# Kernel optimization log

Hardware: AMD Instinct MI355X
Metric: run time of the kernel (lower is better)

The kernel has to match this reference:

```python
import jax, jax.numpy as jnp
import numpy as np

NEG_SLOPE = 0.2  # PyG GATConv default negative_slope
NUM_GRAPHS = 64


def gat_conv(x, src, dst, W, a_src, a_dst, bias, concat):
    """PyG-style GATConv (eval mode, self-loops already appended to src/dst)."""
    N = x.shape[0]
    H, C = a_src.shape
    h = (x @ W).reshape(N, H, C)                      # [N,H,C]
    al_s = jnp.sum(h * a_src, axis=-1)                # [N,H]
    al_d = jnp.sum(h * a_dst, axis=-1)                # [N,H]
    e = jax.nn.leaky_relu(al_s[src] + al_d[dst], NEG_SLOPE)  # [E,H]
    # numerically-stable segment softmax over incoming edges of each dst node
    m = jax.ops.segment_max(e, dst, num_segments=N)   # [N,H]
    ex = jnp.exp(e - m[dst])
    denom = jax.ops.segment_sum(ex, dst, num_segments=N)
    alpha = ex / (denom[dst] + 1e-16)                 # [E,H]
    out = jax.ops.segment_sum(h[src] * alpha[:, :, None], dst, num_segments=N)  # [N,H,C]
    out = out.reshape(N, H * C) if concat else out.mean(axis=1)
    return out + bias


def setup_inputs() -> dict:
    key = jax.random.key(0)
    ks = jax.random.split(key, 32)
    N, E, F_in, H = 20000, 100000, 128, 8
    x = jax.random.normal(ks[0], (N, F_in), jnp.float32)
    edge_index = jax.random.randint(ks[1], (2, E), 0, N, dtype=jnp.int32)
    batch = jnp.sort(jax.random.randint(ks[2], (N,), 0, NUM_GRAPHS, dtype=jnp.int32))
    inp = {"x": x, "edge_index": edge_index, "batch": batch}
    # (fan_in, per-head channels) for conv1..conv_final
    dims = [(F_in, 64), (512, 256), (2048, 256), (2048, 256), (2048, 256)]
    ki = 3
    for i, (fi, c) in enumerate(dims, 1):
        concat = i < 5
        inp[f"W{i}"] = jax.random.normal(ks[ki], (fi, H * c), jnp.float32) * (1.0 / np.sqrt(fi)); ki += 1
        inp[f"a_src{i}"] = jax.random.normal(ks[ki], (H, c), jnp.float32) * 0.1; ki += 1
        inp[f"a_dst{i}"] = jax.random.normal(ks[ki], (H, c), jnp.float32) * 0.1; ki += 1
        inp[f"b{i}"] = jnp.zeros((H * c if concat else c,), jnp.float32)
    inp["W_lin"] = jax.random.normal(ks[ki], (256, 128), jnp.float32) * (1.0 / np.sqrt(256))
    inp["b_lin"] = jnp.zeros((128,), jnp.float32)
    return inp


def reference(x, edge_index, batch,
              W1, a_src1, a_dst1, b1,
              W2, a_src2, a_dst2, b2,
              W3, a_src3, a_dst3, b3,
              W4, a_src4, a_dst4, b4,
              W5, a_src5, a_dst5, b5,
              W_lin, b_lin):
    N = x.shape[0]
    loop = jnp.arange(N, dtype=edge_index.dtype)  # GATConv add_self_loops=True
    src = jnp.concatenate([edge_index[0], loop])
    dst = jnp.concatenate([edge_index[1], loop])
    h = jax.nn.elu(gat_conv(x, src, dst, W1, a_src1, a_dst1, b1, True))
    h = jax.nn.elu(gat_conv(h, src, dst, W2, a_src2, a_dst2, b2, True))
    h = jax.nn.elu(gat_conv(h, src, dst, W3, a_src3, a_dst3, b3, True))
    h = jax.nn.elu(gat_conv(h, src, dst, W4, a_src4, a_dst4, b4, True))
    h = jax.nn.elu(gat_conv(h, src, dst, W5, a_src5, a_dst5, b5, False))
    sums = jax.ops.segment_sum(h, batch, num_segments=NUM_GRAPHS)
    counts = jax.ops.segment_sum(jnp.ones((N, 1), h.dtype), batch, num_segments=NUM_GRAPHS)
    pooled = jax.nn.elu(sums / jnp.maximum(counts, 1.0))  # global_mean_pool + elu
    return pooled @ W_lin + b_lin
```

## Files before the change

kernel.cpp:

```cpp
#include <hip/hip_runtime.h>
#include <hip/hip_fp16.h>
#include <math.h>

#define NHEADS 8
#define NG 64

typedef _Float16 half8_t __attribute__((ext_vector_type(8)));
typedef _Float16 half4_t __attribute__((ext_vector_type(4)));
typedef float    float4_t __attribute__((ext_vector_type(4)));
typedef __attribute__((address_space(1))) const void g_void;
typedef __attribute__((address_space(3))) void l_void;

__device__ __forceinline__ float elu_f(float x)   { return x > 0.f ? x : expf(x) - 1.f; }
__device__ __forceinline__ float lrelu_f(float x) { return x >= 0.f ? x : 0.2f * x; }

__device__ __forceinline__ float4 ld4(const float* p) { return *(const float4*)p; }
__device__ __forceinline__ float4 ld4(const __half* p) {
    const __half2* q = (const __half2*)p;
    __half2 a = q[0], b = q[1];
    return make_float4(__half2float(a.x), __half2float(a.y),
                       __half2float(b.x), __half2float(b.y));
}
__device__ __forceinline__ void st4(float* p, float4 v) { *(float4*)p = v; }
__device__ __forceinline__ void st4(__half* p, float4 v) {
    __half2 a, b;
    a.x = __float2half(v.x); a.y = __float2half(v.y);
    b.x = __float2half(v.z); b.y = __float2half(v.w);
    __half2* q = (__half2*)p; q[0] = a; q[1] = b;
}
__device__ __forceinline__ float scl(float v)  { return v; }
__device__ __forceinline__ float scl(__half v) { return __half2float(v); }
__device__ __forceinline__ void sst(float* p, float v)  { *p = v; }
__device__ __forceinline__ void sst(__half* p, float v) { *p = __float2half(v); }

struct h4s { __half a, b, c, d; };

__global__ void hist_kernel(const int* __restrict__ ei, int E, int Etot, int* __restrict__ counts) {
    int e = blockIdx.x * blockDim.x + threadIdx.x;
    if (e >= Etot) return;
    int dst = (e < E) ? ei[E + e] : (e - E);
    atomicAdd(&counts[dst], 1);
}

__global__ __launch_bounds__(256) void scan_kernel(const int* __restrict__ counts,
                                                   int* __restrict__ offsets,
                                                   int* __restrict__ cursor, int N) {
    __shared__ int wsum[4];
    const int tid = threadIdx.x;
    const int lane = tid & 63, wid = tid >> 6;
    int carry = 0;
    for (int base = 0; base < N; base += 1024) {
        int i0 = base + tid * 4;
        int v0 = 0, v1 = 0, v2 = 0, v3 = 0;
        if (i0 + 3 < N) {
            int4 q = *(const int4*)(counts + i0);
            v0 = q.x; v1 = q.y; v2 = q.z; v3 = q.w;
        } else {
            if (i0     < N) v0 = counts[i0];
            if (i0 + 1 < N) v1 = counts[i0 + 1];
            if (i0 + 2 < N) v2 = counts[i0 + 2];
            if (i0 + 3 < N) v3 = counts[i0 + 3];
        }
        int tsum = v0 + v1 + v2 + v3;
        int incl = tsum;
#pragma unroll
        for (int off = 1; off < 64; off <<= 1) {
            int t = __shfl_up(incl, off);
            if (lane >= off) incl += t;
        }
        if (lane == 63) wsum[wid] = incl;
        __syncthreads();
        int woff = carry;
        for (int w = 0; w < wid; ++w) woff += wsum[w];
        int o0 = woff + incl - tsum;
        int o1 = o0 + v0, o2 = o1 + v1, o3 = o2 + v2;
        if (i0     < N) { offsets[i0]     = o0; cursor[i0]     = o0; }
        if (i0 + 1 < N) { offsets[i0 + 1] = o1; cursor[i0 + 1] = o1; }
        if (i0 + 2 < N) { offsets[i0 + 2] = o2; cursor[i0 + 2] = o2; }
        if (i0 + 3 < N) { offsets[i0 + 3] = o3; cursor[i0 + 3] = o3; }
        __syncthreads();
        carry += wsum[0] + wsum[1] + wsum[2] + wsum[3];
    }
    if (tid == 0) offsets[N] = carry;
}

__global__ void scatter_kernel(const int* __restrict__ ei, int E, int Etot,
                               int* __restrict__ cursor, int* __restrict__ perm_src) {
    int e = blockIdx.x * blockDim.x + threadIdx.x;
    if (e >= Etot) return;
    int src, dst;
    if (e < E) { src = ei[e]; dst = ei[E + e]; }
    else       { src = e - E; dst = e - E; }
    int pos = atomicAdd(&cursor[dst], 1);
    perm_src[pos] = src;
}

struct PrepArgs {
    const float* x; __half* x16; long n4;
    const float* W0; const float* W1; const float* W2; const float* W3; const float* W4;
    __half* T0; __half* T1; __half* T2; __half* T3; __half* T4;
    int K0, K1, K2, K3, K4;
    int N0, N1, N2, N3, N4;
    int b0, b1, b2, b3, b4, b5;
};

__global__ __launch_bounds__(256) void prep_kernel(PrepArgs a) {
    int bid = blockIdx.x;
    if (bid < a.b0) {
        long i = (long)bid * 256 + threadIdx.x;
        if (i < a.n4) {
            float4 v = ((const float4*)a.x)[i];
            h4s o; o.a = __float2half(v.x); o.b = __float2half(v.y);
            o.c = __float2half(v.z); o.d = __float2half(v.w);
            ((h4s*)a.x16)[i] = o;
        }
        return;
    }
    const float* W; __half* T; int K, Nn, t;
    if      (bid < a.b1) { W = a.W0; T = a.T0; K = a.K0; Nn = a.N0; t = bid - a.b0; }
    else if (bid < a.b2) { W = a.W1; T = a.T1; K = a.K1; Nn = a.N1; t = bid - a.b1; }
    else if (bid < a.b3) { W = a.W2; T = a.T2; K = a.K2; Nn = a.N2; t = bid - a.b2; }
    else if (bid < a.b4) { W = a.W3; T = a.T3; K = a.K3; Nn = a.N3; t = bid - a.b3; }
    else                 { W = a.W4; T = a.T4; K = a.K4; Nn = a.N4; t = bid - a.b4; }
    int tilesx = Nn >> 5;
    int nb = (t % tilesx) * 32, kb = (t / tilesx) * 32;
    __shared__ float tt[32][33];
    int tx = threadIdx.x & 31, ty = threadIdx.x >> 5;
#pragma unroll
    for (int r = 0; r < 32; r += 8)
        tt[ty + r][tx] = W[(size_t)(kb + ty + r) * Nn + nb + tx];
    __syncthreads();
#pragma unroll
    for (int r = 0; r < 32; r += 8)
        T[(size_t)(nb + ty + r) * K + kb + tx] = __float2half(tt[tx][ty + r]);
}

__global__ __launch_bounds__(256) void gemm_mfma_kernel(const __half* __restrict__ A,
                                                        const __half* __restrict__ Bt,
                                                        __half* __restrict__ C,
                                                        int M, int N, int K) {
    __shared__ __align__(16) __half Asm[128 * 64];
    __shared__ __align__(16) __half Bsm[128 * 64];
    const int tid  = threadIdx.x;
    const int lane = tid & 63;
    const int wave = tid >> 6;

    const int nwg = (int)(gridDim.x * gridDim.y);
    const int lin = (int)(blockIdx.y * gridDim.x + blockIdx.x);
    const int q = nwg >> 3, r = nwg & 7;
    const int xcd = lin & 7, idx = lin >> 3;
    const int nid = (xcd < r ? xcd * (q + 1) : r * (q + 1) + (xcd - r) * q) + idx;
    const int bx = nid % (int)gridDim.x;
    const int by = nid / (int)gridDim.x;
    const int row0 = by * 128;
    const int col0 = bx * 128;

    const int l15 = lane & 15;
    const int l4  = lane >> 4;
    const int wm  = (wave >> 1) * 64;
    const int wn  = (wave & 1) * 64;

    const int sl_row = lane >> 3;
    const int sl_kch = (lane & 7) ^ sl_row;

    float4_t acc[4][4];
#pragma unroll
    for (int i = 0; i < 4; ++i)
#pragma unroll
        for (int j = 0; j < 4; ++j)
            acc[i][j] = (float4_t){0.f, 0.f, 0.f, 0.f};

    for (int k0 = 0; k0 < K; k0 += 64) {
#pragma unroll
        for (int i = 0; i < 4; ++i) {
            int rr = (i * 4 + wave) * 8 + sl_row;
            int ar = row0 + rr; if (ar >= M) ar = M - 1;
            const __half* ga = A + (size_t)ar * K + k0 + sl_kch * 8;
            char* la = (char*)Asm + ((i * 4 + wave) * 1024 + lane * 16);
            __builtin_amdgcn_global_load_lds((g_void*)ga, (l_void*)la, 16, 0, 0);
            const __half* gb = Bt + (size_t)(col0 + rr) * K + k0 + sl_kch * 8;
            char* lb = (char*)Bsm + ((i * 4 + wave) * 1024 + lane * 16);
            __builtin_amdgcn_global_load_lds((g_void*)gb, (l_void*)lb, 16, 0, 0);
        }
        __syncthreads();
#pragma unroll
        for (int kh = 0; kh < 2; ++kh) {
            half8_t af[4], bf[4];
#pragma unroll
            for (int f = 0; f < 4; ++f) {
                int rowa = wm + f * 16 + l15;
                int ca = (kh * 4 + l4) ^ (rowa & 7);
                af[f] = *(const half8_t*)((const char*)Asm + rowa * 128 + ca * 16);
                int rowb = wn + f * 16 + l15;
                int cb = (kh * 4 + l4) ^ (rowb & 7);
                bf[f] = *(const half8_t*)((const char*)Bsm + rowb * 128 + cb * 16);
            }
#pragma unroll
            for (int fm = 0; fm < 4; ++fm)
#pragma unroll
                for (int fn = 0; fn < 4; ++fn)
                    acc[fm][fn] = __builtin_amdgcn_mfma_f32_16x16x32_f16(af[fm], bf[fn], acc[fm][fn], 0, 0, 0);
        }
        __syncthreads();
    }

#pragma unroll
    for (int fm = 0; fm < 4; ++fm) {
#pragma unroll
        for (int r2 = 0; r2 < 4; ++r2) {
            int row = row0 + wm + fm * 16 + l4 * 4 + r2;
            if (row < M) {
#pragma unroll
                for (int fn = 0; fn < 4; ++fn) {
                    int col = col0 + wn + fn * 16 + l15;
                    C[(size_t)row * N + col] = __float2half(acc[fm][fn][r2]);
                }
            }
        }
    }
}

template <typename TA, typename TC>
__global__ __launch_bounds__(256) void gemm_kernel(const TA* __restrict__ A,
                                                   const float* __restrict__ B,
                                                   TC* __restrict__ C,
                                                   int M, int N, int K) {
    __shared__ float As[16][64];
    __shared__ float Bs[16][64];
    const int tid  = threadIdx.x;
    const int row0 = blockIdx.y * 64, col0 = blockIdx.x * 64;
    const int am = tid >> 2, ak = (tid & 3) << 2;
    const int bk = tid >> 4, bn = (tid & 15) << 2;
    const int ty = (tid >> 4) << 2, tx = (tid & 15) << 2;
    float acc[4][4] = {};
    const int arow = row0 + am;
    for (int k0 = 0; k0 < K; k0 += 16) {
        float4 a4 = make_float4(0.f, 0.f, 0.f, 0.f);
        if (arow < M) a4 = ld4(A + (size_t)arow * K + k0 + ak);
        As[ak + 0][am] = a4.x; As[ak + 1][am] = a4.y;
        As[ak + 2][am] = a4.z; As[ak + 3][am] = a4.w;
        *(float4*)&Bs[bk][bn] = *(const float4*)(B + (size_t)(k0 + bk) * N + col0 + bn);
        __syncthreads();
#pragma unroll
        for (int k = 0; k < 16; ++k) {
            float4 ar = *(const float4*)&As[k][ty];
            float4 br = *(const float4*)&Bs[k][tx];
            acc[0][0] += ar.x * br.x; acc[0][1] += ar.x * br.y; acc[0][2] += ar.x * br.z; acc[0][3] += ar.x * br.w;
            acc[1][0] += ar.y * br.x; acc[1][1] += ar.y * br.y; acc[1][2] += ar.y * br.z; acc[1][3] += ar.y * br.w;
            acc[2][0] += ar.z * br.x; acc[2][1] += ar.z * br.y; acc[2][2] += ar.z * br.z; acc[2][3] += ar.z * br.w;
            acc[3][0] += ar.w * br.x; acc[3][1] += ar.w * br.y; acc[3][2] += ar.w * br.z; acc[3][3] += ar.w * br.w;
        }
        __syncthreads();
    }
#pragma unroll
    for (int i = 0; i < 4; ++i) {
        int r = row0 + ty + i;
        if (r < M) {
            float4 o = make_float4(acc[i][0], acc[i][1], acc[i][2], acc[i][3]);
            st4(C + (size_t)r * N + col0 + tx, o);
        }
    }
}

template <int C>
__global__ void al_vec_kernel(const __half* __restrict__ ht, const float* __restrict__ a_src,
                              const float* __restrict__ a_dst, float* __restrict__ al_s,
                              float* __restrict__ al_d, int N) {
    int wid  = (int)((blockIdx.x * blockDim.x + threadIdx.x) >> 6);
    int lane = threadIdx.x & 63;
    if (wid >= N * NHEADS) return;
    int n = wid / NHEADS, h = wid % NHEADS;
    float ss = 0.f, sd = 0.f;
    int c0 = lane * 4;
    if (c0 < C) {
        const __half* hp = ht + (size_t)n * (NHEADS * C) + h * C + c0;
        half4_t v = *(const half4_t*)hp;
        float4 as4 = *(const float4*)(a_src + h * C + c0);
        float4 ad4 = *(const float4*)(a_dst + h * C + c0);
        float v0 = (float)v[0], v1 = (float)v[1], v2 = (float)v[2], v3 = (float)v[3];
        ss = v0 * as4.x + v1 * as4.y + v2 * as4.z + v3 * as4.w;
        sd = v0 * ad4.x + v1 * ad4.y + v2 * ad4.z + v3 * ad4.w;
    }
#pragma unroll
    for (int off = 32; off > 0; off >>= 1) {
        ss += __shfl_down(ss, off);
        sd += __shfl_down(sd, off);
    }
    if (lane == 0) { al_s[wid] = ss; al_d[wid] = sd; }
}

__global__ __launch_bounds__(256) void alpha_wave_kernel(const int* __restrict__ offsets,
                                                         const int* __restrict__ perm_src,
                                                         const float* __restrict__ al_s,
                                                         const float* __restrict__ al_d,
                                                         float* __restrict__ alpha,
                                                         float* __restrict__ inv_d, int N) {
    int wid  = (int)((blockIdx.x * blockDim.x + threadIdx.x) >> 6);
    int lane = threadIdx.x & 63;
    if (wid >= N) return;
    int n = wid;
    int h = lane & 7, es = lane >> 3;
    int s = offsets[n], e = offsets[n + 1];
    float ad = al_d[(size_t)n * 8 + h];
    float m = -1e30f;
    for (int p0 = s; p0 < e; p0 += 8) {
        int p = p0 + es;
        if (p < e) {
            int src = perm_src[p];
            m = fmaxf(m, lrelu_f(al_s[(size_t)src * 8 + h] + ad));
        }
    }
#pragma unroll
    for (int off = 8; off < 64; off <<= 1) m = fmaxf(m, __shfl_xor(m, off));
    float den = 0.f;
    for (int p0 = s; p0 < e; p0 += 8) {
        int p = p0 + es;
        if (p < e) {
            int src = perm_src[p];
            float ex = expf(lrelu_f(al_s[(size_t)src * 8 + h] + ad) - m);
            alpha[(size_t)p * 8 + h] = ex;
            den += ex;
        }
    }
#pragma unroll
    for (int off = 8; off < 64; off <<= 1) den += __shfl_xor(den, off);
    if (es == 0) inv_d[(size_t)n * 8 + h] = 1.f / (den + 1e-16f);
}

template <int HC, int C, int MODE>
__global__ __launch_bounds__(256) void agg_vec_kernel(const __half* __restrict__ ht,
                                                      const float* __restrict__ alpha,
                                                      const float* __restrict__ inv_d,
                                                      const int* __restrict__ offsets,
                                                      const int* __restrict__ perm_src,
                                                      const float* __restrict__ bias,
                                                      void* __restrict__ outv, int N) {
    constexpr int V = HC / 256;
    int n = blockIdx.x;
    int tid = threadIdx.x;
    const int head = (tid * V) / C;
    float acc[V];
#pragma unroll
    for (int i = 0; i < V; ++i) acc[i] = 0.f;
    int s = offsets[n], e = offsets[n + 1];
    const __half* base = ht + (size_t)tid * V;
    const float* ap = alpha + head;
    int p = s;
    for (; p + 4 <= e; p += 4) {
        int s0 = perm_src[p], s1 = perm_src[p + 1], s2 = perm_src[p + 2], s3 = perm_src[p + 3];
        float a0 = ap[(size_t)p * 8],       a1 = ap[(size_t)(p + 1) * 8];
        float a2 = ap[(size_t)(p + 2) * 8], a3 = ap[(size_t)(p + 3) * 8];
        if (V == 8) {
            half8_t v0 = *(const half8_t*)(base + (size_t)s0 * HC);
            half8_t v1 = *(const half8_t*)(base + (size_t)s1 * HC);
            half8_t v2 = *(const half8_t*)(base + (size_t)s2 * HC);
            half8_t v3 = *(const half8_t*)(base + (size_t)s3 * HC);
#pragma unroll
            for (int i = 0; i < 8; ++i) acc[i] += a0 * (float)v0[i];
#pragma unroll
            for (int i = 0; i < 8; ++i) acc[i] += a1 * (float)v1[i];
#pragma unroll
            for (int i = 0; i < 8; ++i) acc[i] += a2 * (float)v2[i];
#pragma unroll
            for (int i = 0; i < 8; ++i) acc[i] += a3 * (float)v3[i];
        } else {
            __half2 w0 = *(const __half2*)(base + (size_t)s0 * HC);
            __half2 w1 = *(const __half2*)(base + (size_t)s1 * HC);
            __half2 w2 = *(const __half2*)(base + (size_t)s2 * HC);
            __half2 w3 = *(const __half2*)(base + (size_t)s3 * HC);
            acc[0] += a0 * __half2float(w0.x); acc[1] += a0 * __half2float(w0.y);
            acc[0] += a1 * __half2float(w1.x); acc[1] += a1 * __half2float(w1.y);
            acc[0] += a2 * __half2float(w2.x); acc[1] += a2 * __half2float(w2.y);
            acc[0] += a3 * __half2float(w3.x); acc[1] += a3 * __half2float(w3.y);
        }
    }
    for (; p < e; ++p) {
        int src = perm_src[p];
        float a = ap[(size_t)p * 8];
        const __half* hp = base + (size_t)src * HC;
        if (V == 8) {
            half8_t v = *(const half8_t*)hp;
#pragma unroll
            for (int i = 0; i < 8; ++i) acc[i] += a * (float)v[i];
        } else {
            __half2 v2 = *(const __half2*)hp;
            acc[0] += a * __half2float(v2.x);
            acc[1] += a * __half2float(v2.y);
        }
    }
    float inv = inv_d[(size_t)n * NHEADS + head];
    if (MODE == 0) {
        __half* out = (__half*)outv;
        if (V == 8) {
            half8_t o;
#pragma unroll
            for (int i = 0; i < 8; ++i)
                o[i] = (_Float16)elu_f(acc[i] * inv + bias[tid * 8 + i]);
            *(half8_t*)(out + (size_t)n * HC + tid * 8) = o;
        } else {
            __half2 o;
            o.x = __float2half(elu_f(acc[0] * inv + bias[tid * 2 + 0]));
            o.y = __float2half(elu_f(acc[1] * inv + bias[tid * 2 + 1]));
            *(__half2*)(out + (size_t)n * HC + tid * 2) = o;
        }
    } else {
        __shared__ float sm[256][8];
#pragma unroll
        for (int i = 0; i < 8; ++i) sm[tid][i] = acc[i] * inv;
        __syncthreads();
        float ssum = 0.f;
#pragma unroll
        for (int h = 0; h < 8; ++h) ssum += sm[h * 32 + (tid >> 3)][tid & 7];
        float* out = (float*)outv;
        out[(size_t)n * C + tid] = elu_f(ssum * (1.f / NHEADS) + bias[tid]);
    }
}

template <typename TH>
__global__ void al_kernel(const TH* __restrict__ ht, const float* __restrict__ a_src,
                          const float* __restrict__ a_dst, float* __restrict__ al_s,
                          float* __restrict__ al_d, int N, int C) {
    int wid  = (int)((blockIdx.x * blockDim.x + threadIdx.x) >> 6);
    int lane = threadIdx.x & 63;
    if (wid >= N * NHEADS) return;
    int n = wid / NHEADS, h = wid % NHEADS;
    const TH* hp = ht + (size_t)n * (NHEADS * C) + h * C;
    float ss = 0.f, sd = 0.f;
    for (int c = lane; c < C; c += 64) {
        float v = scl(hp[c]);
        ss += v * a_src[h * C + c];
        sd += v * a_dst[h * C + c];
    }
#pragma unroll
    for (int off = 32; off > 0; off >>= 1) {
        ss += __shfl_down(ss, off);
        sd += __shfl_down(sd, off);
    }
    if (lane == 0) { al_s[wid] = ss; al_d[wid] = sd; }
}

__global__ void alpha_kernel(const int* __restrict__ offsets, const int* __restrict__ perm_src,
                             const float* __restrict__ al_s, const float* __restrict__ al_d,
                             float* __restrict__ alpha, int N) {
    int idx = blockIdx.x * blockDim.x + threadIdx.x;
    if (idx >= N * NHEADS) return;
    int n = idx / NHEADS, h = idx % NHEADS;
    int s = offsets[n], e = offsets[n + 1];
    float ad = al_d[idx];
    float m = -1e30f;
    for (int p = s; p < e; ++p) {
        float v = lrelu_f(al_s[perm_src[p] * NHEADS + h] + ad);
        m = fmaxf(m, v);
    }
    float denom = 0.f;
    for (int p = s; p < e; ++p) {
        float v  = lrelu_f(al_s[perm_src[p] * NHEADS + h] + ad);
        float ex = expf(v - m);
        alpha[(size_t)p * NHEADS + h] = ex;
        denom += ex;
    }
    float inv = 1.f / (denom + 1e-16f);
    for (int p = s; p < e; ++p) alpha[(size_t)p * NHEADS + h] *= inv;
}

template <int HC, int C, int MODE, typename TH, typename TO>
__global__ __launch_bounds__(256) void agg_kernel(const TH* __restrict__ ht,
                                                  const float* __restrict__ alpha,
                                                  const int* __restrict__ offsets,
                                                  const int* __restrict__ perm_src,
                                                  const float* __restrict__ bias,
                                                  TO* __restrict__ out, int N) {
    constexpr int PER = HC / 256;
    int n = blockIdx.x;
    int tid = threadIdx.x;
    float acc[PER];
#pragma unroll
    for (int i = 0; i < PER; ++i) acc[i] = 0.f;
    int s = offsets[n], e = offsets[n + 1];
    for (int p = s; p < e; ++p) {
        int src = perm_src[p];
        const TH* hp = ht + (size_t)src * HC;
#pragma unroll
        for (int i = 0; i < PER; ++i) {
            int j = tid + i * 256;
            float a = alpha[(size_t)p * NHEADS + (j / C)];
            acc[i] += a * scl(hp[j]);
        }
    }
    if (MODE == 0) {
#pragma unroll
        for (int i = 0; i < PER; ++i) {
            int j = tid + i * 256;
            sst(&out[(size_t)n * HC + j], elu_f(acc[i] + bias[j]));
        }
    } else {
        float srow = 0.f;
#pragma unroll
        for (int i = 0; i < PER; ++i) srow += acc[i];
        sst(&out[(size_t)n * C + tid], elu_f(srow * (1.f / NHEADS) + bias[tid]));
    }
}

__global__ void gstart_kernel(const int* __restrict__ batch, int* __restrict__ gstart, int N) {
    int n = blockIdx.x * blockDim.x + threadIdx.x;
    if (n > N) return;
    if (n == 0) {
        int b0 = batch[0];
        for (int g = 0; g <= b0; ++g) gstart[g] = 0;
    } else if (n == N) {
        int bl = batch[N - 1];
        for (int g = bl + 1; g <= NG; ++g) gstart[g] = N;
    } else {
        int bp = batch[n - 1], bc = batch[n];
        for (int g = bp + 1; g <= bc; ++g) gstart[g] = n;
    }
}

__global__ void pool_kernel(const float* __restrict__ h5, const int* __restrict__ gstart,
                            float* __restrict__ pooled) {
    int g = blockIdx.x, c = threadIdx.x;
    int s = gstart[g], e = gstart[g + 1];
    float sum = 0.f;
    for (int n = s; n < e; ++n) sum += h5[(size_t)n * 256 + c];
    float cnt = fmaxf((float)(e - s), 1.f);
    pooled[g * 256 + c] = elu_f(sum / cnt);
}

__global__ void linear_kernel(const float* __restrict__ pooled, const float* __restrict__ W,
                              const float* __restrict__ b, float* __restrict__ out) {
    int g = blockIdx.x, c = threadIdx.x;
    float s = b[c];
    for (int k = 0; k < 256; ++k) s += pooled[g * 256 + k] * W[k * 128 + c];
    out[g * 128 + c] = s;
}

__device__ __forceinline__ int lb_dev(const int* a, int n, int key) {
    int lo = 0, hi = n;
    while (lo < hi) { int mid = (lo + hi) >> 1; if (a[mid] < key) lo = mid + 1; else hi = mid; }
    return lo;
}

__global__ __launch_bounds__(256) void pool_linear_kernel(const float* __restrict__ h5,
                                                          const int* __restrict__ batch, int N,
                                                          const float* __restrict__ Wlin,
                                                          const float* __restrict__ blin,
                                                          float* __restrict__ out) {
    int g = blockIdx.x, c = threadIdx.x;
    int s = lb_dev(batch, N, g);
    int e = lb_dev(batch, N, g + 1);
    __shared__ float pooled_s[256];
    float sum = 0.f;
    for (int n = s; n < e; ++n) sum += h5[(size_t)n * 256 + c];
    float cnt = fmaxf((float)(e - s), 1.f);
    pooled_s[c] = elu_f(sum / cnt);
    __syncthreads();
    if (c < 128) {
        float acc = blin[c];
        for (int k = 0; k < 256; ++k) acc += pooled_s[k] * Wlin[k * 128 + c];
        out[g * 128 + c] = acc;
    }
}

template <typename TIO, typename TH>
static void run_pipeline(const float* x, const float* const* W, const float* const* asrc,
                         const float* const* adst, const float* const* bias,
                         char* rawIO, char* rawHT,
                         float* al_s, float* al_d, float* alpha_buf,
                         const int* offsets, const int* perm_src,
                         int N, hipStream_t stream) {
    TIO* bufIO = (TIO*)rawIO;
    TH*  bufHT = (TH*)rawHT;
    {
        dim3 g(512 / 64, (N + 63) / 64);
        gemm_kernel<float, TH><<<g, 256, 0, stream>>>(x, W[0], bufHT, N, 512, 128);
        al_kernel<TH><<<(N * NHEADS * 64 + 255) / 256, 256, 0, stream>>>(bufHT, asrc[0], adst[0], al_s, al_d, N, 64);
        alpha_kernel<<<(N * NHEADS + 255) / 256, 256, 0, stream>>>(offsets, perm_src, al_s, al_d, alpha_buf, N);
        agg_kernel<512, 64, 0, TH, TIO><<<N, 256, 0, stream>>>(bufHT, alpha_buf, offsets, perm_src, bias[0], bufIO, N);
    }
    int Kdim = 512;
    for (int l = 1; l < 5; ++l) {
        dim3 g(2048 / 64, (N + 63) / 64);
        gemm_kernel<TIO, TH><<<g, 256, 0, stream>>>(bufIO, W[l], bufHT, N, 2048, Kdim);
        al_kernel<TH><<<(N * NHEADS * 64 + 255) / 256, 256, 0, stream>>>(bufHT, asrc[l], adst[l], al_s, al_d, N, 256);
        alpha_kernel<<<(N * NHEADS + 255) / 256, 256, 0, stream>>>(offsets, perm_src, al_s, al_d, alpha_buf, N);
        if (l < 4)
            agg_kernel<2048, 256, 0, TH, TIO><<<N, 256, 0, stream>>>(bufHT, alpha_buf, offsets, perm_src, bias[l], bufIO, N);
        else
            agg_kernel<2048, 256, 1, TH, float><<<N, 256, 0, stream>>>(bufHT, alpha_buf, offsets, perm_src, bias[l], (float*)rawIO, N);
        Kdim = 2048;
    }
}

extern "C" void kernel_launch(void* const* d_in, const int* in_sizes, int n_in,
                              void* d_out, int out_size, void* d_ws, size_t ws_size,
                              hipStream_t stream) {
    const float* x     = (const float*)d_in[0];
    const int*   ei    = (const int*)d_in[1];
    const int*   batch = (const int*)d_in[2];
    const float* W[5]    = {(const float*)d_in[3],  (const float*)d_in[7],  (const float*)d_in[11],
                            (const float*)d_in[15], (const float*)d_in[19]};
    const float* asrc[5] = {(const float*)d_in[4],  (const float*)d_in[8],  (const float*)d_in[12],
                            (const float*)d_in[16], (const float*)d_in[20]};
    const float* adst[5] = {(const float*)d_in[5],  (const float*)d_in[9],  (const float*)d_in[13],
                            (const float*)d_in[17], (const float*)d_in[21]};
    const float* bias[5] = {(const float*)d_in[6],  (const float*)d_in[10], (const float*)d_in[14],
                            (const float*)d_in[18], (const float*)d_in[22]};
    const float* Wlin = (const float*)d_in[23];
    const float* blin = (const float*)d_in[24];

    const int N    = in_sizes[0] / 128;
    const int E    = in_sizes[1] / 2;
    const int Etot = E + N;

    auto align256 = [](size_t b) { return (b + 255) & ~(size_t)255; };

    size_t sz_counts = align256((size_t)N * 4);
    size_t sz_off    = align256((size_t)(N + 1) * 4);
    size_t sz_cur    = align256((size_t)N * 4);
    size_t sz_perm   = align256((size_t)Etot * 4);
    size_t sz_al     = align256((size_t)N * NHEADS * 4);
    size_t sz_alpha  = align256((size_t)Etot * NHEADS * 4);
    size_t sz_inv    = align256((size_t)N * NHEADS * 4);
    size_t sz_gst    = align256((size_t)(NG + 1) * 4);
    size_t sz_pool   = align256((size_t)NG * 256 * 4);
    size_t misc = sz_counts + sz_off + sz_cur + sz_perm + 2 * sz_al + sz_alpha + sz_inv + sz_gst + sz_pool;

    size_t bigf  = align256((size_t)N * 2048 * sizeof(float));
    size_t bigh  = align256((size_t)N * 2048 * sizeof(__half));
    const int Kd[5] = {128, 512, 2048, 2048, 2048};
    const int Nd[5] = {512, 2048, 2048, 2048, 2048};
    size_t sz_wt_each[5], sz_wt_all = 0;
    for (int l = 0; l < 5; ++l) { sz_wt_each[l] = align256((size_t)Kd[l] * Nd[l] * sizeof(__half)); sz_wt_all += sz_wt_each[l]; }
    size_t sz_x16 = align256((size_t)N * 128 * sizeof(__half));

    int path;
    if      (ws_size >= misc + 2 * bigh + sz_wt_all + sz_x16) path = 3;
    else if (ws_size >= misc + 2 * bigf)                      path = 0;
    else if (ws_size >= misc + bigf + bigh)                   path = 1;
    else if (ws_size >= misc + 2 * bigh)                      path = 2;
    else {
        hipMemsetAsync(d_out, 0, (size_t)out_size * sizeof(float), stream);
        return;
    }

    char* ws = (char*)d_ws;
    size_t off = 0;
    auto carve = [&](size_t bytes) { void* p = ws + off; off += bytes; return p; };
    int*   counts   = (int*)carve(sz_counts);
    int*   offsets  = (int*)carve(sz_off);
    int*   cursor   = (int*)carve(sz_cur);
    int*   perm_src = (int*)carve(sz_perm);
    float* al_s     = (float*)carve(sz_al);
    float* al_d     = (float*)carve(sz_al);
    float* alpha    = (float*)carve(sz_alpha);
    float* inv_d    = (float*)carve(sz_inv);
    int*   gstart   = (int*)carve(sz_gst);
    float* pooled   = (float*)carve(sz_pool);

    hipMemsetAsync(counts, 0, (size_t)N * 4, stream);
    hist_kernel<<<(Etot + 255) / 256, 256, 0, stream>>>(ei, E, Etot, counts);
    scan_kernel<<<1, 256, 0, stream>>>(counts, offsets, cursor, N);
    scatter_kernel<<<(Etot + 255) / 256, 256, 0, stream>>>(ei, E, Etot, cursor, perm_src);

    if (path == 3) {
        char*   rawIO = (char*)carve(bigh);
        char*   rawHT = (char*)carve(bigh);
        __half* Wt[5];
        for (int l = 0; l < 5; ++l) Wt[l] = (__half*)carve(sz_wt_each[l]);
        __half* x16   = (__half*)carve(sz_x16);
        __half* bufIO = (__half*)rawIO;
        __half* bufHT = (__half*)rawHT;

        PrepArgs pa;
        pa.x = x; pa.x16 = x16; pa.n4 = (long)N * 128 / 4;
        pa.W0 = W[0]; pa.W1 = W[1]; pa.W2 = W[2]; pa.W3 = W[3]; pa.W4 = W[4];
        pa.T0 = Wt[0]; pa.T1 = Wt[1]; pa.T2 = Wt[2]; pa.T3 = Wt[3]; pa.T4 = Wt[4];
        pa.K0 = Kd[0]; pa.K1 = Kd[1]; pa.K2 = Kd[2]; pa.K3 = Kd[3]; pa.K4 = Kd[4];
        pa.N0 = Nd[0]; pa.N1 = Nd[1]; pa.N2 = Nd[2]; pa.N3 = Nd[3]; pa.N4 = Nd[4];
        int bacc = (int)((pa.n4 + 255) / 256);
        pa.b0 = bacc;
        int bends[5];
        for (int l = 0; l < 5; ++l) { bacc += (Nd[l] / 32) * (Kd[l] / 32); bends[l] = bacc; }
        pa.b1 = bends[0]; pa.b2 = bends[1]; pa.b3 = bends[2]; pa.b4 = bends[3]; pa.b5 = bends[4];
        prep_kernel<<<pa.b5, 256, 0, stream>>>(pa);

        const __half* curA = x16;
        int Kdim = 128;
        for (int l = 0; l < 5; ++l) {
            const int C  = (l == 0) ? 64 : 256;
            const int HC = NHEADS * C;
            {
                dim3 gg(HC / 128, (N + 127) / 128);
                gemm_mfma_kernel<<<gg, 256, 0, stream>>>(curA, Wt[l], bufHT, N, HC, Kdim);
            }
            if (l == 0)
                al_vec_kernel<64><<<(N * NHEADS * 64 + 255) / 256, 256, 0, stream>>>(bufHT, asrc[l], adst[l], al_s, al_d, N);
            else
                al_vec_kernel<256><<<(N * NHEADS * 64 + 255) / 256, 256, 0, stream>>>(bufHT, asrc[l], adst[l], al_s, al_d, N);
            alpha_wave_kernel<<<(N * 64 + 255) / 256, 256, 0, stream>>>(offsets, perm_src, al_s, al_d, alpha, inv_d, N);
            if (l == 0)
                agg_vec_kernel<512, 64, 0><<<N, 256, 0, stream>>>(bufHT, alpha, inv_d, offsets, perm_src, bias[l], bufIO, N);
            else if (l < 4)
                agg_vec_kernel<2048, 256, 0><<<N, 256, 0, stream>>>(bufHT, alpha, inv_d, offsets, perm_src, bias[l], bufIO, N);
            else
                agg_vec_kernel<2048, 256, 1><<<N, 256, 0, stream>>>(bufHT, alpha, inv_d, offsets, perm_src, bias[l], (float*)rawIO, N);
            curA = bufIO;
            Kdim = (l == 0) ? 512 : 2048;
        }
        pool_linear_kernel<<<NG, 256, 0, stream>>>((const float*)rawIO, batch, N, Wlin, blin, (float*)d_out);
        return;
    }

    char* rawIO = (char*)carve(path == 2 ? bigh : bigf);
    char* rawHT = (char*)carve(path == 0 ? bigf : bigh);

    if (path == 0)
        run_pipeline<float, float>(x, W, asrc, adst, bias, rawIO, rawHT, al_s, al_d, alpha, offsets, perm_src, N, stream);
    else if (path == 1)
        run_pipeline<float, __half>(x, W, asrc, adst, bias, rawIO, rawHT, al_s, al_d, alpha, offsets, perm_src, N, stream);
    else
        run_pipeline<__half, __half>(x, W, asrc, adst, bias, rawIO, rawHT, al_s, al_d, alpha, offsets, perm_src, N, stream);

    gstart_kernel<<<(N + 1 + 255) / 256, 256, 0, stream>>>(batch, gstart, N);
    pool_kernel<<<NG, 256, 0, stream>>>((const float*)rawIO, gstart, pooled);
    linear_kernel<<<NG, 128, 0, stream>>>(pooled, Wlin, blin, (float*)d_out);
}
```

Measured before the change: 1.284 ms.

## Fold attention logit projections into GEMM via precomputed W·a vectors

Precomputes W·a_src and W·a_dst per head in the prep kernel and appends them as an extra 16-column MFMA operand in the GEMM. Blocks in the first column tile then emit al_s/al_d directly. This removes the separate al_vec pass that re-read the full N×2048 fp16 feature matrix every layer. The cost is extra MFMAs and uncached global loads in one wave per row tile, possible load imbalance, and a change in numerics from rounding W·a to fp16.

Result: slower. 1.430 ms (+11.4%).

```diff
diff --git a/kernel.cpp b/kernel.cpp
--- a/kernel.cpp
+++ b/kernel.cpp
@@ -97,11 +97,12 @@
 
 struct PrepArgs {
     const float* x; __half* x16; long n4;
-    const float* W0; const float* W1; const float* W2; const float* W3; const float* W4;
-    __half* T0; __half* T1; __half* T2; __half* T3; __half* T4;
-    int K0, K1, K2, K3, K4;
-    int N0, N1, N2, N3, N4;
-    int b0, b1, b2, b3, b4, b5;
+    const float* W[5]; __half* T[5];
+    const float* As[5]; const float* Ad[5]; __half* ALW[5];
+    int K[5], Nn[5];
+    int b0;
+    int tb[5];
+    int ab[5];
 };
 
 __global__ __launch_bounds__(256) void prep_kernel(PrepArgs a) {
@@ -116,28 +117,57 @@
         }
         return;
     }
-    const float* W; __half* T; int K, Nn, t;
-    if      (bid < a.b1) { W = a.W0; T = a.T0; K = a.K0; Nn = a.N0; t = bid - a.b0; }
-    else if (bid < a.b2) { W = a.W1; T = a.T1; K = a.K1; Nn = a.N1; t = bid - a.b1; }
-    else if (bid < a.b3) { W = a.W2; T = a.T2; K = a.K2; Nn = a.N2; t = bid - a.b2; }
-    else if (bid < a.b4) { W = a.W3; T = a.T3; K = a.K3; Nn = a.N3; t = bid - a.b3; }
-    else                 { W = a.W4; T = a.T4; K = a.K4; Nn = a.N4; t = bid - a.b4; }
-    int tilesx = Nn >> 5;
-    int nb = (t % tilesx) * 32, kb = (t / tilesx) * 32;
-    __shared__ float tt[32][33];
-    int tx = threadIdx.x & 31, ty = threadIdx.x >> 5;
-#pragma unroll
-    for (int r = 0; r < 32; r += 8)
-        tt[ty + r][tx] = W[(size_t)(kb + ty + r) * Nn + nb + tx];
-    __syncthreads();
-#pragma unroll
-    for (int r = 0; r < 32; r += 8)
-        T[(size_t)(nb + ty + r) * K + kb + tx] = __float2half(tt[tx][ty + r]);
+    if (bid < a.tb[4]) {
+        int l = 0, base = a.b0;
+#pragma unroll
+        for (int j = 0; j < 5; ++j) if (bid >= a.tb[j]) { l = j + 1; base = a.tb[j]; }
+        const float* W = a.W[l]; __half* T = a.T[l];
+        int K = a.K[l], Nn = a.Nn[l];
+        int t = bid - base;
+        int tilesx = Nn >> 5;
+        int nb = (t % tilesx) * 32, kb = (t / tilesx) * 32;
+        __shared__ float tt[32][33];
+        int tx = threadIdx.x & 31, ty = threadIdx.x >> 5;
+#pragma unroll
+        for (int r = 0; r < 32; r += 8)
+            tt[ty + r][tx] = W[(size_t)(kb + ty + r) * Nn + nb + tx];
+        __syncthreads();
+#pragma unroll
+        for (int r = 0; r < 32; r += 8)
+            T[(size_t)(nb + ty + r) * K + kb + tx] = __float2half(tt[tx][ty + r]);
+        return;
+    }
+    {
+        int l = 0, base = a.tb[4];
+#pragma unroll
+        for (int j = 0; j < 5; ++j) if (bid >= a.ab[j]) { l = j + 1; base = a.ab[j]; }
+        int t = (bid - base) * 256 + threadIdx.x;
+        int K = a.K[l];
+        if (t >= K * 8) return;
+        int k = t >> 3, h = t & 7;
+        int C = a.Nn[l] >> 3;
+        const float* wrow = a.W[l] + (size_t)k * a.Nn[l] + h * C;
+        const float* as = a.As[l] + h * C;
+        const float* ad = a.Ad[l] + h * C;
+        float s1 = 0.f, s2 = 0.f;
+        for (int c = 0; c < C; c += 4) {
+            float4 wv = *(const float4*)(wrow + c);
+            float4 av = *(const float4*)(as + c);
+            float4 dv = *(const float4*)(ad + c);
+            s1 += wv.x * av.x + wv.y * av.y + wv.z * av.z + wv.w * av.w;
+            s2 += wv.x * dv.x + wv.y * dv.y + wv.z * dv.z + wv.w * dv.w;
+        }
+        a.ALW[l][(size_t)h * K + k]       = __float2half(s1);
+        a.ALW[l][(size_t)(8 + h) * K + k] = __float2half(s2);
+    }
 }
 
 __global__ __launch_bounds__(256) void gemm_mfma_kernel(const __half* __restrict__ A,
                                                         const __half* __restrict__ Bt,
                                                         __half* __restrict__ C,
+                                                        const __half* __restrict__ alw,
+                                                        float* __restrict__ al_s,
+                                                        float* __restrict__ al_d,
                                                         int M, int N, int K) {
     __shared__ __align__(16) __half Asm[128 * 64];
     __shared__ __align__(16) __half Bsm[128 * 64];
@@ -163,12 +193,17 @@
     const int sl_row = lane >> 3;
     const int sl_kch = (lane & 7) ^ sl_row;
 
+    const bool do_al = (col0 == 0) && (wn == 0);
+
     float4_t acc[4][4];
 #pragma unroll
     for (int i = 0; i < 4; ++i)
 #pragma unroll
         for (int j = 0; j < 4; ++j)
             acc[i][j] = (float4_t){0.f, 0.f, 0.f, 0.f};
+    float4_t acc_al[4];
+#pragma unroll
+    for (int i = 0; i < 4; ++i) acc_al[i] = (float4_t){0.f, 0.f, 0.f, 0.f};
 
     for (int k0 = 0; k0 < K; k0 += 64) {
 #pragma unroll
@@ -200,6 +235,12 @@
 #pragma unroll
                 for (int fn = 0; fn < 4; ++fn)
                     acc[fm][fn] = __builtin_amdgcn_mfma_f32_16x16x32_f16(af[fm], bf[fn], acc[fm][fn], 0, 0, 0);
+            if (do_al) {
+                half8_t bal = *(const half8_t*)(alw + (size_t)l15 * K + k0 + kh * 32 + l4 * 8);
+#pragma unroll
+                for (int fm = 0; fm < 4; ++fm)
+                    acc_al[fm] = __builtin_amdgcn_mfma_f32_16x16x32_f16(af[fm], bal, acc_al[fm], 0, 0, 0);
+            }
         }
         __syncthreads();
     }
@@ -214,6 +255,19 @@
                 for (int fn = 0; fn < 4; ++fn) {
                     int col = col0 + wn + fn * 16 + l15;
                     C[(size_t)row * N + col] = __float2half(acc[fm][fn][r2]);
+                }
+            }
+        }
+    }
+    if (do_al) {
+#pragma unroll
+        for (int fm = 0; fm < 4; ++fm) {
+#pragma unroll
+            for (int r2 = 0; r2 < 4; ++r2) {
+                int row = row0 + wm + fm * 16 + l4 * 4 + r2;
+                if (row < M) {
+                    if (l15 < 8) al_s[(size_t)row * 8 + l15]       = acc_al[fm][r2];
+                    else         al_d[(size_t)row * 8 + (l15 - 8)] = acc_al[fm][r2];
                 }
             }
         }
@@ -262,33 +316,6 @@
     }
 }
 
-template <int C>
-__global__ void al_vec_kernel(const __half* __restrict__ ht, const float* __restrict__ a_src,
-                              const float* __restrict__ a_dst, float* __restrict__ al_s,
-                              float* __restrict__ al_d, int N) {
-    int wid  = (int)((blockIdx.x * blockDim.x + threadIdx.x) >> 6);
-    int lane = threadIdx.x & 63;
-    if (wid >= N * NHEADS) return;
-    int n = wid / NHEADS, h = wid % NHEADS;
-    float ss = 0.f, sd = 0.f;
-    int c0 = lane * 4;
-    if (c0 < C) {
-        const __half* hp = ht + (size_t)n * (NHEADS * C) + h * C + c0;
-        half4_t v = *(const half4_t*)hp;
-        float4 as4 = *(const float4*)(a_src + h * C + c0);
-        float4 ad4 = *(const float4*)(a_dst + h * C + c0);
-        float v0 = (float)v[0], v1 = (float)v[1], v2 = (float)v[2], v3 = (float)v[3];
-        ss = v0 * as4.x + v1 * as4.y + v2 * as4.z + v3 * as4.w;
-        sd = v0 * ad4.x + v1 * ad4.y + v2 * ad4.z + v3 * ad4.w;
-    }
-#pragma unroll
-    for (int off = 32; off > 0; off >>= 1) {
-        ss += __shfl_down(ss, off);
-        sd += __shfl_down(sd, off);
-    }
-    if (lane == 0) { al_s[wid] = ss; al_d[wid] = sd; }
-}
-
 __global__ __launch_bounds__(256) void alpha_wave_kernel(const int* __restrict__ offsets,
                                                          const int* __restrict__ perm_src,
                                                          const float* __restrict__ al_s,
@@ -629,15 +656,18 @@
     size_t bigh  = align256((size_t)N * 2048 * sizeof(__half));
     const int Kd[5] = {128, 512, 2048, 2048, 2048};
     const int Nd[5] = {512, 2048, 2048, 2048, 2048};
-    size_t sz_wt_each[5], sz_wt_all = 0;
-    for (int l = 0; l < 5; ++l) { sz_wt_each[l] = align256((size_t)Kd[l] * Nd[l] * sizeof(__half)); sz_wt_all += sz_wt_each[l]; }
+    size_t sz_wt_each[5], sz_wt_all = 0, sz_alw_each[5], sz_alw_all = 0;
+    for (int l = 0; l < 5; ++l) {
+        sz_wt_each[l]  = align256((size_t)Kd[l] * Nd[l] * sizeof(__half)); sz_wt_all += sz_wt_each[l];
+        sz_alw_each[l] = align256((size_t)16 * Kd[l] * sizeof(__half));    sz_alw_all += sz_alw_each[l];
+    }
     size_t sz_x16 = align256((size_t)N * 128 * sizeof(__half));
 
     int path;
-    if      (ws_size >= misc + 2 * bigh + sz_wt_all + sz_x16) path = 3;
-    else if (ws_size >= misc + 2 * bigf)                      path = 0;
-    else if (ws_size >= misc + bigf + bigh)                   path = 1;
-    else if (ws_size >= misc + 2 * bigh)                      path = 2;
+    if      (ws_size >= misc + 2 * bigh + sz_wt_all + sz_alw_all + sz_x16) path = 3;
+    else if (ws_size >= misc + 2 * bigf)                                   path = 0;
+    else if (ws_size >= misc + bigf + bigh)                                path = 1;
+    else if (ws_size >= misc + 2 * bigh)                                   path = 2;
     else {
         hipMemsetAsync(d_out, 0, (size_t)out_size * sizeof(float), stream);
         return;
@@ -665,24 +695,24 @@
     if (path == 3) {
         char*   rawIO = (char*)carve(bigh);
         char*   rawHT = (char*)carve(bigh);
-        __half* Wt[5];
-        for (int l = 0; l < 5; ++l) Wt[l] = (__half*)carve(sz_wt_each[l]);
+        __half* Wt[5];  for (int l = 0; l < 5; ++l) Wt[l]  = (__half*)carve(sz_wt_each[l]);
+        __half* ALW[5]; for (int l = 0; l < 5; ++l) ALW[l] = (__half*)carve(sz_alw_each[l]);
         __half* x16   = (__half*)carve(sz_x16);
         __half* bufIO = (__half*)rawIO;
         __half* bufHT = (__half*)rawHT;
 
         PrepArgs pa;
         pa.x = x; pa.x16 = x16; pa.n4 = (long)N * 128 / 4;
-        pa.W0 = W[0]; pa.W1 = W[1]; pa.W2 = W[2]; pa.W3 = W[3]; pa.W4 = W[4];
-        pa.T0 = Wt[0]; pa.T1 = Wt[1]; pa.T2 = Wt[2]; pa.T3 = Wt[3]; pa.T4 = Wt[4];
-        pa.K0 = Kd[0]; pa.K1 = Kd[1]; pa.K2 = Kd[2]; pa.K3 = Kd[3]; pa.K4 = Kd[4];
-        pa.N0 = Nd[0]; pa.N1 = Nd[1]; pa.N2 = Nd[2]; pa.N3 = Nd[3]; pa.N4 = Nd[4];
+        for (int l = 0; l < 5; ++l) {
+            pa.W[l] = W[l]; pa.T[l] = Wt[l];
+            pa.As[l] = asrc[l]; pa.Ad[l] = adst[l]; pa.ALW[l] = ALW[l];
+            pa.K[l] = Kd[l]; pa.Nn[l] = Nd[l];
+        }
         int bacc = (int)((pa.n4 + 255) / 256);
         pa.b0 = bacc;
-        int bends[5];
-        for (int l = 0; l < 5; ++l) { bacc += (Nd[l] / 32) * (Kd[l] / 32); bends[l] = bacc; }
-        pa.b1 = bends[0]; pa.b2 = bends[1]; pa.b3 = bends[2]; pa.b4 = bends[3]; pa.b5 = bends[4];
-        prep_kernel<<<pa.b5, 256, 0, stream>>>(pa);
+        for (int l = 0; l < 5; ++l) { bacc += (Nd[l] / 32) * (Kd[l] / 32); pa.tb[l] = bacc; }
+        for (int l = 0; l < 5; ++l) { bacc += (Kd[l] * 8 + 255) / 256;     pa.ab[l] = bacc; }
+        prep_kernel<<<bacc, 256, 0, stream>>>(pa);
 
         const __half* curA = x16;
         int Kdim = 128;
@@ -691,12 +721,8 @@
             const int HC = NHEADS * C;
             {
                 dim3 gg(HC / 128, (N + 127) / 128);
-                gemm_mfma_kernel<<<gg, 256, 0, stream>>>(curA, Wt[l], bufHT, N, HC, Kdim);
+                gemm_mfma_kernel<<<gg, 256, 0, stream>>>(curA, Wt[l], bufHT, ALW[l], al_s, al_d, N, HC, Kdim);
             }
-            if (l == 0)
-                al_vec_kernel<64><<<(N * NHEADS * 64 + 255) / 256, 256, 0, stream>>>(bufHT, asrc[l], adst[l], al_s, al_d, N);
-            else
-                al_vec_kernel<256><<<(N * NHEADS * 64 + 255) / 256, 256, 0, stream>>>(bufHT, asrc[l], adst[l], al_s, al_d, N);
             alpha_wave_kernel<<<(N * 64 + 255) / 256, 256, 0, stream>>>(offsets, perm_src, al_s, al_d, alpha, inv_d, N);
             if (l == 0)
                 agg_vec_kernel<512, 64, 0><<<N, 256, 0, stream>>>(bufHT, alpha, inv_d, offsets, perm_src, bias[l], bufIO, N);
```

## Fuse segment softmax into aggregation kernel, recomputing attention weights on the fly

Applied to the files above, without the earlier changes.

Removes the separate alpha_wave kernel and the alpha/inv_d buffers. Each wave of the aggregation block now computes the per-node max and denominator itself, and each thread recomputes exp(leaky_relu) per edge while aggregating. This drops one launch per layer and the global write/read of per-edge alpha. In exchange every wave redundantly runs the softmax reductions and every thread does extra exps and gathers of al_s. Also refactors prep kernel args into arrays.

Result: no change. 1.261 ms (-1.7%).

```diff
diff --git a/kernel.cpp b/kernel.cpp
--- a/kernel.cpp
+++ b/kernel.cpp
@@ -97,11 +97,10 @@
 
 struct PrepArgs {
     const float* x; __half* x16; long n4;
-    const float* W0; const float* W1; const float* W2; const float* W3; const float* W4;
-    __half* T0; __half* T1; __half* T2; __half* T3; __half* T4;
-    int K0, K1, K2, K3, K4;
-    int N0, N1, N2, N3, N4;
-    int b0, b1, b2, b3, b4, b5;
+    const float* W[5]; __half* T[5];
+    int K[5], Nn[5];
+    int b0;
+    int tb[5];
 };
 
 __global__ __launch_bounds__(256) void prep_kernel(PrepArgs a) {
@@ -116,12 +115,12 @@
         }
         return;
     }
-    const float* W; __half* T; int K, Nn, t;
-    if      (bid < a.b1) { W = a.W0; T = a.T0; K = a.K0; Nn = a.N0; t = bid - a.b0; }
-    else if (bid < a.b2) { W = a.W1; T = a.T1; K = a.K1; Nn = a.N1; t = bid - a.b1; }
-    else if (bid < a.b3) { W = a.W2; T = a.T2; K = a.K2; Nn = a.N2; t = bid - a.b2; }
-    else if (bid < a.b4) { W = a.W3; T = a.T3; K = a.K3; Nn = a.N3; t = bid - a.b3; }
-    else                 { W = a.W4; T = a.T4; K = a.K4; Nn = a.N4; t = bid - a.b4; }
+    int l = 0, base = a.b0;
+#pragma unroll
+    for (int j = 0; j < 4; ++j) if (bid >= a.tb[j]) { l = j + 1; base = a.tb[j]; }
+    const float* W = a.W[l]; __half* T = a.T[l];
+    int K = a.K[l], Nn = a.Nn[l];
+    int t = bid - base;
     int tilesx = Nn >> 5;
     int nb = (t % tilesx) * 32, kb = (t / tilesx) * 32;
     __shared__ float tt[32][33];
@@ -289,67 +288,49 @@
     if (lane == 0) { al_s[wid] = ss; al_d[wid] = sd; }
 }
 
-__global__ __launch_bounds__(256) void alpha_wave_kernel(const int* __restrict__ offsets,
-                                                         const int* __restrict__ perm_src,
-                                                         const float* __restrict__ al_s,
-                                                         const float* __restrict__ al_d,
-                                                         float* __restrict__ alpha,
-                                                         float* __restrict__ inv_d, int N) {
-    int wid  = (int)((blockIdx.x * blockDim.x + threadIdx.x) >> 6);
-    int lane = threadIdx.x & 63;
-    if (wid >= N) return;
-    int n = wid;
-    int h = lane & 7, es = lane >> 3;
-    int s = offsets[n], e = offsets[n + 1];
-    float ad = al_d[(size_t)n * 8 + h];
-    float m = -1e30f;
-    for (int p0 = s; p0 < e; p0 += 8) {
-        int p = p0 + es;
-        if (p < e) {
-            int src = perm_src[p];
-            m = fmaxf(m, lrelu_f(al_s[(size_t)src * 8 + h] + ad));
-        }
-    }
-#pragma unroll
-    for (int off = 8; off < 64; off <<= 1) m = fmaxf(m, __shfl_xor(m, off));
-    float den = 0.f;
-    for (int p0 = s; p0 < e; p0 += 8) {
-        int p = p0 + es;
-        if (p < e) {
-            int src = perm_src[p];
-            float ex = expf(lrelu_f(al_s[(size_t)src * 8 + h] + ad) - m);
-            alpha[(size_t)p * 8 + h] = ex;
-            den += ex;
-        }
-    }
-#pragma unroll
-    for (int off = 8; off < 64; off <<= 1) den += __shfl_xor(den, off);
-    if (es == 0) inv_d[(size_t)n * 8 + h] = 1.f / (den + 1e-16f);
-}
-
 template <int HC, int C, int MODE>
-__global__ __launch_bounds__(256) void agg_vec_kernel(const __half* __restrict__ ht,
-                                                      const float* __restrict__ alpha,
-                                                      const float* __restrict__ inv_d,
-                                                      const int* __restrict__ offsets,
-                                                      const int* __restrict__ perm_src,
-                                                      const float* __restrict__ bias,
-                                                      void* __restrict__ outv, int N) {
+__global__ __launch_bounds__(256) void agg_fused_kernel(const __half* __restrict__ ht,
+                                                        const float* __restrict__ al_s,
+                                                        const float* __restrict__ al_d,
+                                                        const int* __restrict__ offsets,
+                                                        const int* __restrict__ perm_src,
+                                                        const float* __restrict__ bias,
+                                                        void* __restrict__ outv, int N) {
     constexpr int V = HC / 256;
     int n = blockIdx.x;
     int tid = threadIdx.x;
+    int lane = tid & 63;
     const int head = (tid * V) / C;
+    int s = offsets[n], e = offsets[n + 1];
+
+    int h2 = lane & 7, es = lane >> 3;
+    float ad2 = al_d[(size_t)n * 8 + h2];
+    float m = -1e30f;
+    for (int p0 = s + es; p0 < e; p0 += 8)
+        m = fmaxf(m, lrelu_f(al_s[(size_t)perm_src[p0] * 8 + h2] + ad2));
+#pragma unroll
+    for (int off = 8; off < 64; off <<= 1) m = fmaxf(m, __shfl_xor(m, off));
+    float den = 0.f;
+    for (int p0 = s + es; p0 < e; p0 += 8)
+        den += expf(lrelu_f(al_s[(size_t)perm_src[p0] * 8 + h2] + ad2) - m);
+#pragma unroll
+    for (int off = 8; off < 64; off <<= 1) den += __shfl_xor(den, off);
+    float inv0 = 1.f / (den + 1e-16f);
+    float mh   = __shfl(m, head);
+    float invh = __shfl(inv0, head);
+    float adh  = __shfl(ad2, head);
+
     float acc[V];
 #pragma unroll
     for (int i = 0; i < V; ++i) acc[i] = 0.f;
-    int s = offsets[n], e = offsets[n + 1];
     const __half* base = ht + (size_t)tid * V;
-    const float* ap = alpha + head;
     int p = s;
     for (; p + 4 <= e; p += 4) {
         int s0 = perm_src[p], s1 = perm_src[p + 1], s2 = perm_src[p + 2], s3 = perm_src[p + 3];
-        float a0 = ap[(size_t)p * 8],       a1 = ap[(size_t)(p + 1) * 8];
-        float a2 = ap[(size_t)(p + 2) * 8], a3 = ap[(size_t)(p + 3) * 8];
+        float a0 = expf(lrelu_f(al_s[(size_t)s0 * 8 + head] + adh) - mh);
+        float a1 = expf(lrelu_f(al_s[(size_t)s1 * 8 + head] + adh) - mh);
+        float a2 = expf(lrelu_f(al_s[(size_t)s2 * 8 + head] + adh) - mh);
+        float a3 = expf(lrelu_f(al_s[(size_t)s3 * 8 + head] + adh) - mh);
         if (V == 8) {
             half8_t v0 = *(const half8_t*)(base + (size_t)s0 * HC);
             half8_t v1 = *(const half8_t*)(base + (size_t)s1 * HC);
@@ -376,7 +357,7 @@
     }
     for (; p < e; ++p) {
         int src = perm_src[p];
-        float a = ap[(size_t)p * 8];
+        float a = expf(lrelu_f(al_s[(size_t)src * 8 + head] + adh) - mh);
         const __half* hp = base + (size_t)src * HC;
         if (V == 8) {
             half8_t v = *(const half8_t*)hp;
@@ -388,25 +369,24 @@
             acc[1] += a * __half2float(v2.y);
         }
     }
-    float inv = inv_d[(size_t)n * NHEADS + head];
     if (MODE == 0) {
         __half* out = (__half*)outv;
         if (V == 8) {
             half8_t o;
 #pragma unroll
             for (int i = 0; i < 8; ++i)
-                o[i] = (_Float16)elu_f(acc[i] * inv + bias[tid * 8 + i]);
+                o[i] = (_Float16)elu_f(acc[i] * invh + bias[tid * 8 + i]);
             *(half8_t*)(out + (size_t)n * HC + tid * 8) = o;
         } else {
             __half2 o;
-            o.x = __float2half(elu_f(acc[0] * inv + bias[tid * 2 + 0]));
-            o.y = __float2half(elu_f(acc[1] * inv + bias[tid * 2 + 1]));
+            o.x = __float2half(elu_f(acc[0] * invh + bias[tid * 2 + 0]));
+            o.y = __float2half(elu_f(acc[1] * invh + bias[tid * 2 + 1]));
             *(__half2*)(out + (size_t)n * HC + tid * 2) = o;
         }
     } else {
         __shared__ float sm[256][8];
 #pragma unroll
-        for (int i = 0; i < 8; ++i) sm[tid][i] = acc[i] * inv;
+        for (int i = 0; i < 8; ++i) sm[tid][i] = acc[i] * invh;
         __syncthreads();
         float ssum = 0.f;
 #pragma unroll
@@ -620,10 +600,9 @@
     size_t sz_perm   = align256((size_t)Etot * 4);
     size_t sz_al     = align256((size_t)N * NHEADS * 4);
     size_t sz_alpha  = align256((size_t)Etot * NHEADS * 4);
-    size_t sz_inv    = align256((size_t)N * NHEADS * 4);
     size_t sz_gst    = align256((size_t)(NG + 1) * 4);
     size_t sz_pool   = align256((size_t)NG * 256 * 4);
-    size_t misc = sz_counts + sz_off + sz_cur + sz_perm + 2 * sz_al + sz_alpha + sz_inv + sz_gst + sz_pool;
+    size_t misc = sz_counts + sz_off + sz_cur + sz_perm + 2 * sz_al + sz_alpha + sz_gst + sz_pool;
 
     size_t bigf  = align256((size_t)N * 2048 * sizeof(float));
     size_t bigh  = align256((size_t)N * 2048 * sizeof(__half));
@@ -653,7 +632,6 @@
     float* al_s     = (float*)carve(sz_al);
     float* al_d     = (float*)carve(sz_al);
     float* alpha    = (float*)carve(sz_alpha);
-    float* inv_d    = (float*)carve(sz_inv);
     int*   gstart   = (int*)carve(sz_gst);
     float* pooled   = (float*)carve(sz_pool);
 
@@ -673,16 +651,11 @@
 
         PrepArgs pa;
         pa.x = x; pa.x16 = x16; pa.n4 = (long)N * 128 / 4;
-        pa.W0 = W[0]; pa.W1 = W[1]; pa.W2 = W[2]; pa.W3 = W[3]; pa.W4 = W[4];
-        pa.T0 = Wt[0]; pa.T1 = Wt[1]; pa.T2 = Wt[2]; pa.T3 = Wt[3]; pa.T4 = Wt[4];
-        pa.K0 = Kd[0]; pa.K1 = Kd[1]; pa.K2 = Kd[2]; pa.K3 = Kd[3]; pa.K4 = Kd[4];
-        pa.N0 = Nd[0]; pa.N1 = Nd[1]; pa.N2 = Nd[2]; pa.N3 = Nd[3]; pa.N4 = Nd[4];
+        for (int l = 0; l < 5; ++l) { pa.W[l] = W[l]; pa.T[l] = Wt[l]; pa.K[l] = Kd[l]; pa.Nn[l] = Nd[l]; }
         int bacc = (int)((pa.n4 + 255) / 256);
         pa.b0 = bacc;
-        int bends[5];
-        for (int l = 0; l < 5; ++l) { bacc += (Nd[l] / 32) * (Kd[l] / 32); bends[l] = bacc; }
-        pa.b1 = bends[0]; pa.b2 = bends[1]; pa.b3 = bends[2]; pa.b4 = bends[3]; pa.b5 = bends[4];
-        prep_kernel<<<pa.b5, 256, 0, stream>>>(pa);
+        for (int l = 0; l < 5; ++l) { bacc += (Nd[l] / 32) * (Kd[l] / 32); pa.tb[l] = bacc; }
+        prep_kernel<<<bacc, 256, 0, stream>>>(pa);
 
         const __half* curA = x16;
         int Kdim = 128;
@@ -697,13 +670,12 @@
                 al_vec_kernel<64><<<(N * NHEADS * 64 + 255) / 256, 256, 0, stream>>>(bufHT, asrc[l], adst[l], al_s, al_d, N);
             else
                 al_vec_kernel<256><<<(N * NHEADS * 64 + 255) / 256, 256, 0, stream>>>(bufHT, asrc[l], adst[l], al_s, al_d, N);
-            alpha_wave_kernel<<<(N * 64 + 255) / 256, 256, 0, stream>>>(offsets, perm_src, al_s, al_d, alpha, inv_d, N);
             if (l == 0)
-                agg_vec_kernel<512, 64, 0><<<N, 256, 0, stream>>>(bufHT, alpha, inv_d, offsets, perm_src, bias[l], bufIO, N);
+                agg_fused_kernel<512, 64, 0><<<N, 256, 0, stream>>>(bufHT, al_s, al_d, offsets, perm_src, bias[l], bufIO, N);
             else if (l < 4)
-                agg_vec_kernel<2048, 256, 0><<<N, 256, 0, stream>>>(bufHT, alpha, inv_d, offsets, perm_src, bias[l], bufIO, N);
+                agg_fused_kernel<2048, 256, 0><<<N, 256, 0, stream>>>(bufHT, al_s, al_d, offsets, perm_src, bias[l], bufIO, N);
             else
-                agg_vec_kernel<2048, 256, 1><<<N, 256, 0, stream>>>(bufHT, alpha, inv_d, offsets, perm_src, bias[l], (float*)rawIO, N);
+                agg_fused_kernel<2048, 256, 1><<<N, 256, 0, stream>>>(bufHT, al_s, al_d, offsets, perm_src, bias[l], (float*)rawIO, N);
             curA = bufIO;
             Kdim = (l == 0) ? 512 : 2048;
         }
```
